# Performance work log

Hardware: AMD Instinct MI355X
Metric: run time of the kernel (lower is better)

## Reference

```python
import jax, jax.numpy as jnp
import numpy as np

H = 19  # input_size == hidden_size

def setup_inputs() -> dict:
    key = jax.random.key(0)
    ks = jax.random.split(key, 7)
    seq_len, batch = 2048, 1024
    s = 1.0 / np.sqrt(H)  # PyTorch default uniform(-1/sqrt(H), 1/sqrt(H))
    x = jax.random.normal(ks[0], (seq_len, batch, H), dtype=jnp.float32)
    W_ih = jax.random.uniform(ks[1], (3 * H, H), jnp.float32, -s, s)
    W_hh = jax.random.uniform(ks[2], (3 * H, H), jnp.float32, -s, s)
    b_ih = jax.random.uniform(ks[3], (3 * H,), jnp.float32, -s, s)
    b_hh = jax.random.uniform(ks[4], (3 * H,), jnp.float32, -s, s)
    W_out = jax.random.uniform(ks[5], (1, H), jnp.float32, -s, s)
    b_out = jax.random.uniform(ks[6], (1,), jnp.float32, -s, s)
    return {"x": x, "W_ih": W_ih, "W_hh": W_hh, "b_ih": b_ih,
            "b_hh": b_hh, "W_out": W_out, "b_out": b_out}

def _gru(x, W_ih, W_hh, b_ih, b_hh):
    # Precompute all input projections in one big GEMM: [T, B, 3H]
    xg = jnp.einsum('tbi,gi->tbg', x, W_ih) + b_ih
    Whr, Whz, Whn = W_hh[:H], W_hh[H:2*H], W_hh[2*H:]
    bhr, bhz, bhn = b_hh[:H], b_hh[H:2*H], b_hh[2*H:]
    h0 = jnp.zeros(x.shape[1:2] + (H,), dtype=x.dtype)

    def step(h, xg_t):
        xr, xz, xn = xg_t[:, :H], xg_t[:, H:2*H], xg_t[:, 2*H:]
        r = jax.nn.sigmoid(xr + h @ Whr.T + bhr)
        z = jax.nn.sigmoid(xz + h @ Whz.T + bhz)
        n = jnp.tanh(xn + r * (h @ Whn.T + bhn))
        h_new = (1.0 - z) * n + z * h
        return h_new, h_new

    _, r_out = jax.lax.scan(step, h0, xg)  # r_out: [T, B, H]
    return r_out

def reference(x, W_ih, W_hh, b_ih, b_hh, W_out, b_out):
    r_out = _gru(x, W_ih, W_hh, b_ih, b_hh)
    return r_out @ W_out.T + b_out  # [T, B, 1]
```

## Files before the change

### kernel.cpp

```cpp
#include <hip/hip_runtime.h>
#include <math.h>

#define HH 19
#define NB 1024
#define TT 2048

typedef float v2f __attribute__((ext_vector_type(2)));
typedef unsigned u2 __attribute__((ext_vector_type(2)));

__device__ __forceinline__ float rlf(float v, int l) {
  return __uint_as_float(__builtin_amdgcn_readlane(__float_as_uint(v), l));
}
__device__ __forceinline__ float frcp(float v) {
  return __builtin_amdgcn_rcpf(v);
}
__device__ __forceinline__ float fexp2(float v) {
#if __has_builtin(__builtin_amdgcn_exp2f)
  return __builtin_amdgcn_exp2f(v);
#else
  return exp2f(v);
#endif
}
__device__ __forceinline__ v2f vfma(v2f a, v2f b, v2f c) {
#if __has_builtin(__builtin_elementwise_fma)
  return __builtin_elementwise_fma(a, b, c);
#else
  v2f r; r.x = fmaf(a.x, b.x, c.x); r.y = fmaf(a.y, b.y, c.y); return r;
#endif
}

#if __has_builtin(__builtin_amdgcn_permlane32_swap)
#define HAVE_PLS 1
__device__ __forceinline__ u2 pls(float x) {
  unsigned u = __float_as_uint(x);
  return __builtin_amdgcn_permlane32_swap(u, u, false, false);
}
#else
#define HAVE_PLS 0
#endif

__global__ void __launch_bounds__(64)
__attribute__((amdgpu_waves_per_eu(1, 1)))
gru57_v4(const float* __restrict__ x, const float* __restrict__ Wih,
         const float* __restrict__ Whh, const float* __restrict__ bih,
         const float* __restrict__ bhh, const float* __restrict__ Wout,
         const float* __restrict__ bout, float* __restrict__ out)
{
  const int b = blockIdx.x;
  const int lane = threadIdx.x;

  const float L2E = 1.4426950408889634f;

  int row;
  if (lane < 32)      row = lane;
  else if (lane < 51) row = lane + 6;
  else if (lane < 57) row = lane - 19;
  else                row = 37;
  const bool isn = (row >= 2 * HH);
  const float scale = isn ? (2.0f * L2E) : L2E;

  v2f wx2[10], wh2[10], wo2[10];
#pragma unroll
  for (int j = 0; j < 10; ++j) {
    const int k0 = 2 * j, k1 = 2 * j + 1;
    wx2[j].x = Wih[row * HH + k0] * scale;
    wx2[j].y = (k1 < HH) ? Wih[row * HH + k1] * scale : 0.0f;
    wh2[j].x = Whh[row * HH + k0] * scale;
    wh2[j].y = (k1 < HH) ? Whh[row * HH + k1] * scale : 0.0f;
    wo2[j].x = Wout[k0];
    wo2[j].y = (k1 < HH) ? Wout[k1] : 0.0f;
  }
  const float bxv = bih[row] * scale, bhv = bhh[row] * scale;
  const float ax0 = isn ? bxv : (bxv + bhv);
  const float ah0 = isn ? bhv : 0.0f;
  const float bo  = bout[0];

  const int il = lane < HH ? lane : HH - 1;
  const int zaddr = ((il < 13) ? (19 + il) : (38 + il)) * 4;

#if HAVE_PLS
  bool loIsX;
  {
    unsigned l = (unsigned)lane;
    u2 pr = __builtin_amdgcn_permlane32_swap(l, l, false, false);
    loIsX = ((unsigned)__builtin_amdgcn_readlane((int)pr.x, 32) < 32u);
  }
#else
  const int loaddr = (lane & 31) * 4;
  const int hiaddr = ((lane & 31) | 32) * 4;
#endif

  float h = 0.0f;
  v2f sh2[10];
#pragma unroll
  for (int j = 0; j < 10; ++j) { sh2[j].x = 0.0f; sh2[j].y = 0.0f; }

  const int kx = lane < HH ? lane : HH - 1;
  const float* __restrict__ xbase = x + (size_t)b * HH + kx;

#define LOADX(dst, trow) do {                                           \
    dst = xbase[(size_t)(trow) * (NB * HH)];                            \
  } while (0)

#define XBCAST(slot, xu) do {                                           \
    _Pragma("unroll")                                                   \
    for (int _j = 0; _j < 9; ++_j) {                                    \
      xu[_j].x = rlf(slot, 2 * _j);                                     \
      xu[_j].y = rlf(slot, 2 * _j + 1);                                 \
    }                                                                   \
    xu[9].x = rlf(slot, 18); xu[9].y = 0.0f;                            \
  } while (0)

#define XDOT(xu, dstvar) do {                                           \
    v2f _aA = {ax0, 0.0f}, _aB = {0.0f, 0.0f};                          \
    _Pragma("unroll")                                                   \
    for (int _j = 0; _j < 5; ++_j)  _aA = vfma(xu[_j], wx2[_j], _aA);   \
    _Pragma("unroll")                                                   \
    for (int _j = 5; _j < 10; ++_j) _aB = vfma(xu[_j], wx2[_j], _aB);   \
    const v2f _s = _aA + _aB;                                           \
    dstvar = _s.x + _s.y;                                               \
  } while (0)

#if HAVE_PLS
#define LOBCAST(val, dst) do { u2 _s = pls(val);                        \
    dst = __uint_as_float(loIsX ? _s.x : _s.y); } while (0)
#define HIBCAST(val, dst) do { u2 _s = pls(val);                        \
    dst = __uint_as_float(loIsX ? _s.y : _s.x); } while (0)
#else
#define LOBCAST(val, dst) dst = __uint_as_float((unsigned)              \
    __builtin_amdgcn_ds_bpermute(loaddr, (int)__float_as_uint(val)))
#define HIBCAST(val, dst) dst = __uint_as_float((unsigned)              \
    __builtin_amdgcn_ds_bpermute(hiaddr, (int)__float_as_uint(val)))
#endif

  float xlA, xlB, xlC, xlD;
  LOADX(xlA, 0); LOADX(xlB, 1); LOADX(xlC, 2); LOADX(xlD, 3);

  float prex;
  {
    v2f xu0[10];
    XBCAST(xlA, xu0);
    XDOT(xu0, prex);
  }

#define BODY(tcur, nslot, lslot) do {                                   \
                 \
    v2f ahA = {ah0, 0.0f}, ahB = {0.0f, 0.0f};                          \
    _Pragma("unroll")                                                   \
    for (int _j = 0; _j < 5; ++_j)  ahA = vfma(sh2[_j], wh2[_j], ahA);  \
    _Pragma("unroll")                                                   \
    for (int _j = 5; _j < 10; ++_j) ahB = vfma(sh2[_j], wh2[_j], ahB);  \
               \
    float prexN;                                                        \
    { v2f _xu[10];                                                      \
      XBCAST(nslot, _xu);                                               \
      XDOT(_xu, prexN); }                                               \
    { const int _tl = ((tcur) + 4 < TT) ? (tcur) + 4 : TT - 1;          \
      LOADX(lslot, _tl); }                                              \
                                                   \
    const v2f ahv = ahA + ahB;                                          \
    const float preh = ahv.x + ahv.y;                                   \
    const float pre  = prex + preh;                                     \
    const float sig  = frcp(1.0f + fexp2(-pre));                        \
    const int zzi = __builtin_amdgcn_ds_bpermute(                       \
        zaddr, (int)__float_as_uint(sig));                              \
    float rr; LOBCAST(sig, rr);                                         \
    const float npre = fmaf(rr, preh, prex);                            \
    const float nn = fmaf(-2.0f, frcp(fexp2(npre) + 1.0f), 1.0f);       \
    float nh; HIBCAST(nn, nh);                                          \
    const float zz = __uint_as_float((unsigned)zzi);                    \
    h = fmaf(zz, h - nh, nh);                                           \
                  \
    _Pragma("unroll")                                                   \
    for (int _j = 0; _j < 9; ++_j) {                                    \
      sh2[_j].x = rlf(h, 2 * _j);                                       \
      sh2[_j].y = rlf(h, 2 * _j + 1);                                   \
    }                                                                   \
    sh2[9].x = rlf(h, 18); sh2[9].y = 0.0f;                             \
        \
    v2f oA = {bo, 0.0f}, oB = {0.0f, 0.0f};                             \
    _Pragma("unroll")                                                   \
    for (int _j = 0; _j < 5; ++_j)  oA = vfma(sh2[_j], wo2[_j], oA);    \
    _Pragma("unroll")                                                   \
    for (int _j = 5; _j < 10; ++_j) oB = vfma(sh2[_j], wo2[_j], oB);    \
    const v2f ov = oA + oB;                                             \
    if (lane == 0) out[(size_t)(tcur) * NB + b] = ov.x + ov.y;          \
    prex = prexN;                                                       \
  } while (0)

  for (int t = 0; t < TT; t += 4) {
    BODY(t + 0, xlB, xlA);
    BODY(t + 1, xlC, xlB);
    BODY(t + 2, xlD, xlC);
    BODY(t + 3, xlA, xlD);
  }

#undef LOADX
#undef XBCAST
#undef XDOT
#undef BODY
#undef LOBCAST
#undef HIBCAST
}

extern "C" void kernel_launch(void* const* d_in, const int* in_sizes, int n_in,
                              void* d_out, int out_size, void* d_ws, size_t ws_size,
                              hipStream_t stream) {
  const float* x    = (const float*)d_in[0];
  const float* Wih  = (const float*)d_in[1];
  const float* Whh  = (const float*)d_in[2];
  const float* bih  = (const float*)d_in[3];
  const float* bhh  = (const float*)d_in[4];
  const float* Wout = (const float*)d_in[5];
  const float* bout = (const float*)d_in[6];
  float* out = (float*)d_out;

  gru57_v4<<<dim3(NB), dim3(64), 0, stream>>>(
      x, Wih, Whh, bih, bhh, Wout, bout, out);
}
```

Before: 555.2 us.

## Split input projection into separate fp16 precompute kernel before recurrence

Adds a parallel kernel that computes all input-gate projections for every timestep and batch element and stores them as fp16 in the workspace. The recurrent kernel then loads one precomputed half value per lane per step, which takes the per-step x broadcast and x-dot-product off the serial loop; its prefetch depth grows to 8 steps. The cost is an extra launch and a large intermediate write and read (about 240 MB of fp16). Storing the projections in fp16 also loses precision. The original fused kernel is kept as a fallback when the workspace is too small.

```diff
diff --git a/kernel.cpp b/kernel.cpp
--- a/kernel.cpp
+++ b/kernel.cpp
@@ -2,24 +2,31 @@
 #include <math.h>
 
 #define HH 19
+#define NG 57
+#define GP 20
 #define NB 1024
 #define TT 2048
 
+typedef float v4f __attribute__((ext_vector_type(4)));
+typedef unsigned u2 __attribute__((ext_vector_type(2)));
 typedef float v2f __attribute__((ext_vector_type(2)));
-typedef unsigned u2 __attribute__((ext_vector_type(2)));
 
 __device__ __forceinline__ float rlf(float v, int l) {
   return __uint_as_float(__builtin_amdgcn_readlane(__float_as_uint(v), l));
 }
-__device__ __forceinline__ float frcp(float v) {
-  return __builtin_amdgcn_rcpf(v);
-}
+__device__ __forceinline__ float frcp(float v) { return __builtin_amdgcn_rcpf(v); }
 __device__ __forceinline__ float fexp2(float v) {
 #if __has_builtin(__builtin_amdgcn_exp2f)
   return __builtin_amdgcn_exp2f(v);
 #else
   return exp2f(v);
 #endif
+}
+__device__ __forceinline__ unsigned short f2h(float f) {
+  return __builtin_bit_cast(unsigned short, (_Float16)f);
+}
+__device__ __forceinline__ float h2f(unsigned short u) {
+  return (float)__builtin_bit_cast(_Float16, u);
 }
 __device__ __forceinline__ v2f vfma(v2f a, v2f b, v2f c) {
 #if __has_builtin(__builtin_elementwise_fma)
@@ -38,6 +45,161 @@
 #else
 #define HAVE_PLS 0
 #endif
+
+__global__ __launch_bounds__(256) void xg_proj(
+    const float* __restrict__ x, const float* __restrict__ Wih,
+    const float* __restrict__ bih, const float* __restrict__ bhh,
+    unsigned short* __restrict__ xg)
+{
+  __shared__ __align__(16) float wl[NG][GP];
+  __shared__ float cb[NG];
+  const float L2E = 1.4426950408889634f;
+  for (int idx = threadIdx.x; idx < NG * GP; idx += 256) {
+    const int g = idx / GP, k = idx - g * GP;
+    const float s = (g < 2 * HH) ? L2E : 2.0f * L2E;
+    wl[g][k] = (k < HH) ? Wih[g * HH + k] * s : 0.0f;
+  }
+  if (threadIdx.x < NG) {
+    const int g = threadIdx.x;
+    const float s = (g < 2 * HH) ? L2E : 2.0f * L2E;
+    cb[g] = (bih[g] + (g < 2 * HH ? bhh[g] : 0.0f)) * s;
+  }
+  __syncthreads();
+
+  const size_t tid = (size_t)blockIdx.x * 256 + threadIdx.x;
+  const float* __restrict__ xr = x + tid * HH;
+  float xv[GP];
+#pragma unroll
+  for (int k = 0; k < HH; ++k) xv[k] = xr[k];
+  xv[HH] = 0.0f;
+
+  unsigned short* __restrict__ o = xg + tid * NG;
+#pragma unroll 3
+  for (int g = 0; g < NG; ++g) {
+    float a = cb[g];
+#pragma unroll
+    for (int q = 0; q < GP; q += 4) {
+      const v4f w = *(const v4f*)&wl[g][q];
+      a = fmaf(xv[q + 0], w.x, a);
+      a = fmaf(xv[q + 1], w.y, a);
+      a = fmaf(xv[q + 2], w.z, a);
+      a = fmaf(xv[q + 3], w.w, a);
+    }
+    o[g] = f2h(a);
+  }
+}
+
+__global__ void __launch_bounds__(64)
+__attribute__((amdgpu_waves_per_eu(1, 1)))
+gru_rec(const unsigned short* __restrict__ xg, const float* __restrict__ Whh,
+        const float* __restrict__ bhh, const float* __restrict__ Wout,
+        const float* __restrict__ bout, float* __restrict__ out)
+{
+  const int b = blockIdx.x;
+  const int lane = threadIdx.x;
+  const float L2E = 1.4426950408889634f;
+
+  int row;
+  if (lane < 32)      row = lane;
+  else if (lane < 51) row = lane + 6;
+  else if (lane < 57) row = lane - 19;
+  else                row = 37;
+  const bool isn = (row >= 2 * HH);
+  const float scale = isn ? (2.0f * L2E) : L2E;
+
+  float wh[HH], wo[HH];
+#pragma unroll
+  for (int k = 0; k < HH; ++k) {
+    wh[k] = Whh[row * HH + k] * scale;
+    wo[k] = Wout[k];
+  }
+  const float ah0 = isn ? bhh[row] * scale : 0.0f;
+  const float bo  = bout[0];
+
+  const int il = lane < HH ? lane : HH - 1;
+  const int zaddr = ((il < 13) ? (19 + il) : (38 + il)) * 4;
+
+#if HAVE_PLS
+  bool loIsX;
+  {
+    unsigned l = (unsigned)lane;
+    u2 pr = __builtin_amdgcn_permlane32_swap(l, l, false, false);
+    loIsX = ((unsigned)__builtin_amdgcn_readlane((int)pr.x, 32) < 32u);
+  }
+#define LOBCAST(val, dst) do { u2 _s = pls(val);                        \
+    dst = __uint_as_float(loIsX ? _s.x : _s.y); } while (0)
+#define HIBCAST(val, dst) do { u2 _s = pls(val);                        \
+    dst = __uint_as_float(loIsX ? _s.y : _s.x); } while (0)
+#else
+  const int loaddr = (lane & 31) * 4;
+  const int hiaddr = ((lane & 31) | 32) * 4;
+#define LOBCAST(val, dst) dst = __uint_as_float((unsigned)              \
+    __builtin_amdgcn_ds_bpermute(loaddr, (int)__float_as_uint(val)))
+#define HIBCAST(val, dst) dst = __uint_as_float((unsigned)              \
+    __builtin_amdgcn_ds_bpermute(hiaddr, (int)__float_as_uint(val)))
+#endif
+
+  float h = 0.0f;
+  float sh[HH];
+#pragma unroll
+  for (int k = 0; k < HH; ++k) sh[k] = 0.0f;
+
+  const unsigned short* __restrict__ xb = xg + (size_t)b * NG + row;
+
+#define LOADX(dst, trow) do {                                           \
+    dst = xb[(size_t)(trow) * (NB * NG)];                               \
+  } while (0)
+
+  unsigned short s0, s1, s2, s3, s4, s5, s6, s7;
+  LOADX(s0, 0); LOADX(s1, 1); LOADX(s2, 2); LOADX(s3, 3);
+  LOADX(s4, 4); LOADX(s5, 5); LOADX(s6, 6); LOADX(s7, 7);
+
+#define BODY(tcur, slot) do {                                           \
+    const float xv = h2f(slot);                                         \
+    float a0 = ah0, a1 = 0.0f, a2 = 0.0f, a3 = 0.0f;                    \
+    _Pragma("unroll")                                                   \
+    for (int _k = 0; _k < HH; ++_k) {                                   \
+      if ((_k & 3) == 0) a0 = fmaf(sh[_k], wh[_k], a0);                 \
+      if ((_k & 3) == 1) a1 = fmaf(sh[_k], wh[_k], a1);                 \
+      if ((_k & 3) == 2) a2 = fmaf(sh[_k], wh[_k], a2);                 \
+      if ((_k & 3) == 3) a3 = fmaf(sh[_k], wh[_k], a3);                 \
+    }                                                                   \
+    const float preh = (a0 + a1) + (a2 + a3);                           \
+    const float pre  = xv + preh;                                       \
+    const float sig  = frcp(1.0f + fexp2(-pre));                        \
+    const int zzi = __builtin_amdgcn_ds_bpermute(                       \
+        zaddr, (int)__float_as_uint(sig));                              \
+    float rr; LOBCAST(sig, rr);                                         \
+    const float npre = fmaf(rr, preh, xv);                              \
+    const float nn = fmaf(-2.0f, frcp(fexp2(npre) + 1.0f), 1.0f);       \
+    float nh; HIBCAST(nn, nh);                                          \
+    const float zz = __uint_as_float((unsigned)zzi);                    \
+    h = fmaf(zz, h - nh, nh);                                           \
+    _Pragma("unroll")                                                   \
+    for (int _k = 0; _k < HH; ++_k) sh[_k] = rlf(h, _k);                \
+    float o0 = bo, o1 = 0.0f, o2 = 0.0f, o3 = 0.0f;                     \
+    _Pragma("unroll")                                                   \
+    for (int _k = 0; _k < HH; ++_k) {                                   \
+      if ((_k & 3) == 0) o0 = fmaf(sh[_k], wo[_k], o0);                 \
+      if ((_k & 3) == 1) o1 = fmaf(sh[_k], wo[_k], o1);                 \
+      if ((_k & 3) == 2) o2 = fmaf(sh[_k], wo[_k], o2);                 \
+      if ((_k & 3) == 3) o3 = fmaf(sh[_k], wo[_k], o3);                 \
+    }                                                                   \
+    if (lane == 0) out[(size_t)(tcur) * NB + b] = (o0 + o1) + (o2 + o3);\
+    { const int _tl = ((tcur) + 8 < TT) ? (tcur) + 8 : TT - 1;          \
+      LOADX(slot, _tl); }                                               \
+  } while (0)
+
+  for (int t = 0; t < TT; t += 8) {
+    BODY(t + 0, s0); BODY(t + 1, s1); BODY(t + 2, s2); BODY(t + 3, s3);
+    BODY(t + 4, s4); BODY(t + 5, s5); BODY(t + 6, s6); BODY(t + 7, s7);
+  }
+
+#undef LOADX
+#undef BODY
+#undef LOBCAST
+#undef HIBCAST
+}
 
 __global__ void __launch_bounds__(64)
 __attribute__((amdgpu_waves_per_eu(1, 1)))
@@ -48,7 +210,6 @@
 {
   const int b = blockIdx.x;
   const int lane = threadIdx.x;
-
   const float L2E = 1.4426950408889634f;
 
   int row;
@@ -85,9 +246,17 @@
     u2 pr = __builtin_amdgcn_permlane32_swap(l, l, false, false);
     loIsX = ((unsigned)__builtin_amdgcn_readlane((int)pr.x, 32) < 32u);
   }
+#define LOBCAST(val, dst) do { u2 _s = pls(val);                        \
+    dst = __uint_as_float(loIsX ? _s.x : _s.y); } while (0)
+#define HIBCAST(val, dst) do { u2 _s = pls(val);                        \
+    dst = __uint_as_float(loIsX ? _s.y : _s.x); } while (0)
 #else
   const int loaddr = (lane & 31) * 4;
   const int hiaddr = ((lane & 31) | 32) * 4;
+#define LOBCAST(val, dst) dst = __uint_as_float((unsigned)              \
+    __builtin_amdgcn_ds_bpermute(loaddr, (int)__float_as_uint(val)))
+#define HIBCAST(val, dst) dst = __uint_as_float((unsigned)              \
+    __builtin_amdgcn_ds_bpermute(hiaddr, (int)__float_as_uint(val)))
 #endif
 
   float h = 0.0f;
@@ -98,10 +267,7 @@
   const int kx = lane < HH ? lane : HH - 1;
   const float* __restrict__ xbase = x + (size_t)b * HH + kx;
 
-#define LOADX(dst, trow) do {                                           \
-    dst = xbase[(size_t)(trow) * (NB * HH)];                            \
-  } while (0)
-
+#define LOADXF(dst, trow) do { dst = xbase[(size_t)(trow) * (NB * HH)]; } while (0)
 #define XBCAST(slot, xu) do {                                           \
     _Pragma("unroll")                                                   \
     for (int _j = 0; _j < 9; ++_j) {                                    \
@@ -110,7 +276,6 @@
     }                                                                   \
     xu[9].x = rlf(slot, 18); xu[9].y = 0.0f;                            \
   } while (0)
-
 #define XDOT(xu, dstvar) do {                                           \
     v2f _aA = {ax0, 0.0f}, _aB = {0.0f, 0.0f};                          \
     _Pragma("unroll")                                                   \
@@ -121,43 +286,21 @@
     dstvar = _s.x + _s.y;                                               \
   } while (0)
 
-#if HAVE_PLS
-#define LOBCAST(val, dst) do { u2 _s = pls(val);                        \
-    dst = __uint_as_float(loIsX ? _s.x : _s.y); } while (0)
-#define HIBCAST(val, dst) do { u2 _s = pls(val);                        \
-    dst = __uint_as_float(loIsX ? _s.y : _s.x); } while (0)
-#else
-#define LOBCAST(val, dst) dst = __uint_as_float((unsigned)              \
-    __builtin_amdgcn_ds_bpermute(loaddr, (int)__float_as_uint(val)))
-#define HIBCAST(val, dst) dst = __uint_as_float((unsigned)              \
-    __builtin_amdgcn_ds_bpermute(hiaddr, (int)__float_as_uint(val)))
-#endif
-
   float xlA, xlB, xlC, xlD;
-  LOADX(xlA, 0); LOADX(xlB, 1); LOADX(xlC, 2); LOADX(xlD, 3);
-
+  LOADXF(xlA, 0); LOADXF(xlB, 1); LOADXF(xlC, 2); LOADXF(xlD, 3);
   float prex;
-  {
-    v2f xu0[10];
-    XBCAST(xlA, xu0);
-    XDOT(xu0, prex);
-  }
-
-#define BODY(tcur, nslot, lslot) do {                                   \
-                 \
+  { v2f xu0[10]; XBCAST(xlA, xu0); XDOT(xu0, prex); }
+
+#define BODYF(tcur, nslot, lslot) do {                                  \
     v2f ahA = {ah0, 0.0f}, ahB = {0.0f, 0.0f};                          \
     _Pragma("unroll")                                                   \
     for (int _j = 0; _j < 5; ++_j)  ahA = vfma(sh2[_j], wh2[_j], ahA);  \
     _Pragma("unroll")                                                   \
     for (int _j = 5; _j < 10; ++_j) ahB = vfma(sh2[_j], wh2[_j], ahB);  \
-               \
     float prexN;                                                        \
-    { v2f _xu[10];                                                      \
-      XBCAST(nslot, _xu);                                               \
-      XDOT(_xu, prexN); }                                               \
+    { v2f _xu[10]; XBCAST(nslot, _xu); XDOT(_xu, prexN); }              \
     { const int _tl = ((tcur) + 4 < TT) ? (tcur) + 4 : TT - 1;          \
-      LOADX(lslot, _tl); }                                              \
-                                                   \
+      LOADXF(lslot, _tl); }                                             \
     const v2f ahv = ahA + ahB;                                          \
     const float preh = ahv.x + ahv.y;                                   \
     const float pre  = prex + preh;                                     \
@@ -170,14 +313,12 @@
     float nh; HIBCAST(nn, nh);                                          \
     const float zz = __uint_as_float((unsigned)zzi);                    \
     h = fmaf(zz, h - nh, nh);                                           \
-                  \
     _Pragma("unroll")                                                   \
     for (int _j = 0; _j < 9; ++_j) {                                    \
       sh2[_j].x = rlf(h, 2 * _j);                                       \
       sh2[_j].y = rlf(h, 2 * _j + 1);                                   \
     }                                                                   \
     sh2[9].x = rlf(h, 18); sh2[9].y = 0.0f;                             \
-        \
     v2f oA = {bo, 0.0f}, oB = {0.0f, 0.0f};                             \
     _Pragma("unroll")                                                   \
     for (int _j = 0; _j < 5; ++_j)  oA = vfma(sh2[_j], wo2[_j], oA);    \
@@ -189,16 +330,16 @@
   } while (0)
 
   for (int t = 0; t < TT; t += 4) {
-    BODY(t + 0, xlB, xlA);
-    BODY(t + 1, xlC, xlB);
-    BODY(t + 2, xlD, xlC);
-    BODY(t + 3, xlA, xlD);
-  }
-
-#undef LOADX
+    BODYF(t + 0, xlB, xlA);
+    BODYF(t + 1, xlC, xlB);
+    BODYF(t + 2, xlD, xlC);
+    BODYF(t + 3, xlA, xlD);
+  }
+
+#undef LOADXF
 #undef XBCAST
 #undef XDOT
-#undef BODY
+#undef BODYF
 #undef LOBCAST
 #undef HIBCAST
 }
@@ -215,6 +356,15 @@
   const float* bout = (const float*)d_in[6];
   float* out = (float*)d_out;
 
-  gru57_v4<<<dim3(NB), dim3(64), 0, stream>>>(
-      x, Wih, Whh, bih, bhh, Wout, bout, out);
-}
+  const size_t need = (size_t)TT * NB * NG * sizeof(unsigned short);
+  if (ws_size >= need) {
+    unsigned short* xgws = (unsigned short*)d_ws;
+    xg_proj<<<dim3((TT * NB) / 256), dim3(256), 0, stream>>>(
+        x, Wih, bih, bhh, xgws);
+    gru_rec<<<dim3(NB), dim3(64), 0, stream>>>(
+        xgws, Whh, bhh, Wout, bout, out);
+  } else {
+    gru57_v4<<<dim3(NB), dim3(64), 0, stream>>>(
+        x, Wih, Whh, bih, bhh, Wout, bout, out);
+  }
+}
```

After: 837.2 us. 1.51x slower.

## Split GRU into fp16 input-projection pass and lane-per-hidden recurrence kernel

Applied to the files above, without the earlier changes.

Adds a separate kernel that precomputes the scaled input projections for all timesteps and stores them in fp16 in the workspace. A new recurrence kernel then assigns one lane per hidden unit, computing all three gates in that lane. It broadcasts h through shared memory with vector loads instead of 19 readlanes, and drops the cross-lane permutes for r, z and n. This takes the x·W_ih dot product and its broadcasts off the serial per-step critical path. In exchange it adds a large workspace write and read, fp16 rounding of the preactivations, and more FMAs per lane.

```diff
diff --git a/kernel.cpp b/kernel.cpp
--- a/kernel.cpp
+++ b/kernel.cpp
@@ -2,18 +2,18 @@
 #include <math.h>
 
 #define HH 19
+#define NG 57
 #define NB 1024
 #define TT 2048
 
 typedef float v2f __attribute__((ext_vector_type(2)));
+typedef float v4f __attribute__((ext_vector_type(4)));
 typedef unsigned u2 __attribute__((ext_vector_type(2)));
 
 __device__ __forceinline__ float rlf(float v, int l) {
   return __uint_as_float(__builtin_amdgcn_readlane(__float_as_uint(v), l));
 }
-__device__ __forceinline__ float frcp(float v) {
-  return __builtin_amdgcn_rcpf(v);
-}
+__device__ __forceinline__ float frcp(float v) { return __builtin_amdgcn_rcpf(v); }
 __device__ __forceinline__ float fexp2(float v) {
 #if __has_builtin(__builtin_amdgcn_exp2f)
   return __builtin_amdgcn_exp2f(v);
@@ -21,6 +21,13 @@
   return exp2f(v);
 #endif
 }
+__device__ __forceinline__ unsigned short f2h(float f) {
+  return __builtin_bit_cast(unsigned short, (_Float16)f);
+}
+__device__ __forceinline__ float h2f(unsigned short u) {
+  return (float)__builtin_bit_cast(_Float16, u);
+}
+__device__ __forceinline__ v2f mk2(float a, float b) { v2f r; r.x = a; r.y = b; return r; }
 __device__ __forceinline__ v2f vfma(v2f a, v2f b, v2f c) {
 #if __has_builtin(__builtin_elementwise_fma)
   return __builtin_elementwise_fma(a, b, c);
@@ -38,6 +45,166 @@
 #else
 #define HAVE_PLS 0
 #endif
+
+__global__ __launch_bounds__(256) void xg_proj2(
+    const float* __restrict__ x, const float* __restrict__ Wih,
+    const float* __restrict__ bih, const float* __restrict__ bhh,
+    unsigned short* __restrict__ xg)
+{
+  const int lane = threadIdx.x & 63;
+  const int wv = __builtin_amdgcn_readfirstlane((int)(threadIdx.x >> 6));
+  const int g = lane < NG ? lane : NG - 1;
+  const float L2E = 1.4426950408889634f;
+  const float scale = (g < 2 * HH) ? -L2E : 2.0f * L2E;
+
+  float w[HH];
+#pragma unroll
+  for (int k = 0; k < HH; ++k) w[k] = Wih[g * HH + k] * scale;
+  const float cbv = (bih[g] + (g < 2 * HH ? bhh[g] : 0.0f)) * scale;
+
+  const size_t pair0 = ((size_t)blockIdx.x * 4 + wv) * 64;
+  for (int p = 0; p < 64; ++p) {
+    const size_t pair = pair0 + p;
+    const float* __restrict__ xr = x + pair * HH;
+    float a = cbv;
+#pragma unroll
+    for (int k = 0; k < HH; ++k) a = fmaf(xr[k], w[k], a);
+    if (lane < NG) xg[pair * NG + g] = f2h(a);
+  }
+}
+
+__global__ void __launch_bounds__(64)
+__attribute__((amdgpu_waves_per_eu(1, 1)))
+gru_rec2(const unsigned short* __restrict__ xg, const float* __restrict__ Whh,
+         const float* __restrict__ bhh, const float* __restrict__ Wout,
+         const float* __restrict__ bout, float* __restrict__ out)
+{
+  __shared__ __align__(16) float hsh[64];
+  const int b = blockIdx.x;
+  const int lane = threadIdx.x;
+  const int i = lane < HH ? lane : HH - 1;
+  const float L2E = 1.4426950408889634f;
+
+  v2f wr2[10], wz2[10], wn2[10], wo2[10];
+#pragma unroll
+  for (int j = 0; j < 10; ++j) {
+    const int k0 = 2 * j, k1 = 2 * j + 1;
+    wr2[j].x = -L2E * Whh[i * HH + k0];
+    wr2[j].y = (k1 < HH) ? -L2E * Whh[i * HH + k1] : 0.0f;
+    wz2[j].x = -L2E * Whh[(HH + i) * HH + k0];
+    wz2[j].y = (k1 < HH) ? -L2E * Whh[(HH + i) * HH + k1] : 0.0f;
+    wn2[j].x = 2.0f * L2E * Whh[(2 * HH + i) * HH + k0];
+    wn2[j].y = (k1 < HH) ? 2.0f * L2E * Whh[(2 * HH + i) * HH + k1] : 0.0f;
+    wo2[j].x = Wout[k0];
+    wo2[j].y = (k1 < HH) ? Wout[k1] : 0.0f;
+  }
+  const float bnv = 2.0f * L2E * bhh[2 * HH + i];
+  const float bo = bout[0];
+
+  float h = 0.0f;
+
+  const unsigned short* __restrict__ xb = xg + (size_t)b * NG;
+#define LR(dst, t) dst = xb[(size_t)(t) * (NB * NG) + i]
+#define LZ(dst, t) dst = xb[(size_t)(t) * (NB * NG) + HH + i]
+#define LN(dst, t) dst = xb[(size_t)(t) * (NB * NG) + 2 * HH + i]
+
+  unsigned short r0,r1,r2,r3,r4,r5,r6,r7;
+  unsigned short z0,z1,z2,z3,z4,z5,z6,z7;
+  unsigned short n0,n1,n2,n3,n4,n5,n6,n7;
+  LR(r0,0); LZ(z0,0); LN(n0,0);  LR(r1,1); LZ(z1,1); LN(n1,1);
+  LR(r2,2); LZ(z2,2); LN(n2,2);  LR(r3,3); LZ(z3,3); LN(n3,3);
+  LR(r4,4); LZ(z4,4); LN(n4,4);  LR(r5,5); LZ(z5,5); LN(n5,5);
+  LR(r6,6); LZ(z6,6); LN(n6,6);  LR(r7,7); LZ(z7,7); LN(n7,7);
+
+#define BODY(tcur, rs, zs, ns) do {                                      \
+              \
+    hsh[lane] = (lane < HH) ? h : 0.0f;                                  \
+    const v4f q0 = *(const v4f*)&hsh[0];                                 \
+    const v4f q1 = *(const v4f*)&hsh[4];                                 \
+    const v4f q2 = *(const v4f*)&hsh[8];                                 \
+    const v4f q3 = *(const v4f*)&hsh[12];                                \
+    const v4f q4 = *(const v4f*)&hsh[16];                                \
+    v2f sh2[10];                                                         \
+    sh2[0]=mk2(q0.x,q0.y); sh2[1]=mk2(q0.z,q0.w);                        \
+    sh2[2]=mk2(q1.x,q1.y); sh2[3]=mk2(q1.z,q1.w);                        \
+    sh2[4]=mk2(q2.x,q2.y); sh2[5]=mk2(q2.z,q2.w);                        \
+    sh2[6]=mk2(q3.x,q3.y); sh2[7]=mk2(q3.z,q3.w);                        \
+    sh2[8]=mk2(q4.x,q4.y); sh2[9]=mk2(q4.z,q4.w);                        \
+                        \
+    v2f oA = mk2(bo, 0.0f), oB = mk2(0.0f, 0.0f);                        \
+    _Pragma("unroll")                                                    \
+    for (int _j = 0; _j < 5; ++_j)  oA = vfma(sh2[_j], wo2[_j], oA);     \
+    _Pragma("unroll")                                                    \
+    for (int _j = 5; _j < 10; ++_j) oB = vfma(sh2[_j], wo2[_j], oB);     \
+    const v2f ov = oA + oB;                                              \
+    if (lane == 0) {                                                     \
+      const int tp = (tcur) > 0 ? (tcur) - 1 : 0;                        \
+      out[(size_t)tp * NB + b] = ov.x + ov.y;                            \
+    }                                                                    \
+                     \
+    const float xvr = h2f(rs), xvz = h2f(zs), xvn = h2f(ns);             \
+    v2f aR0 = mk2(xvr, 0.0f), aR1 = mk2(0.0f, 0.0f);                     \
+    v2f aZ0 = mk2(xvz, 0.0f), aZ1 = mk2(0.0f, 0.0f);                     \
+    v2f aN0 = mk2(bnv, 0.0f), aN1 = mk2(0.0f, 0.0f);                     \
+    _Pragma("unroll")                                                    \
+    for (int _j = 0; _j < 5; ++_j) {                                     \
+      aR0 = vfma(sh2[_j], wr2[_j], aR0);                                 \
+      aZ0 = vfma(sh2[_j], wz2[_j], aZ0);                                 \
+      aN0 = vfma(sh2[_j], wn2[_j], aN0);                                 \
+    }                                                                    \
+    _Pragma("unroll")                                                    \
+    for (int _j = 5; _j < 10; ++_j) {                                    \
+      aR1 = vfma(sh2[_j], wr2[_j], aR1);                                 \
+      aZ1 = vfma(sh2[_j], wz2[_j], aZ1);                                 \
+      aN1 = vfma(sh2[_j], wn2[_j], aN1);                                 \
+    }                                                                    \
+    const v2f mR = aR0 + aR1, mZ = aZ0 + aZ1, mN = aN0 + aN1;            \
+    const float preR = mR.x + mR.y;            \
+    const float preZ = mZ.x + mZ.y;            \
+    const float preN = mN.x + mN.y;          \
+    const float rr = frcp(fexp2(preR) + 1.0f);              \
+    const float zz = frcp(fexp2(preZ) + 1.0f);                           \
+    const float argP = fmaf(rr, preN, xvn);           \
+    const float D = frcp(fexp2(argP) + 1.0f);                            \
+    const float nn = fmaf(-2.0f, D, 1.0f);               \
+    h = fmaf(zz, h - nn, nn);                                            \
+    { const int tl = ((tcur) + 8 < TT) ? (tcur) + 8 : TT - 1;            \
+      LR(rs, tl); LZ(zs, tl); LN(ns, tl); }                              \
+  } while (0)
+
+  for (int t = 0; t < TT; t += 8) {
+    BODY(t + 0, r0, z0, n0); BODY(t + 1, r1, z1, n1);
+    BODY(t + 2, r2, z2, n2); BODY(t + 3, r3, z3, n3);
+    BODY(t + 4, r4, z4, n4); BODY(t + 5, r5, z5, n5);
+    BODY(t + 6, r6, z6, n6); BODY(t + 7, r7, z7, n7);
+  }
+
+  hsh[lane] = (lane < HH) ? h : 0.0f;
+  {
+    const v4f q0 = *(const v4f*)&hsh[0];
+    const v4f q1 = *(const v4f*)&hsh[4];
+    const v4f q2 = *(const v4f*)&hsh[8];
+    const v4f q3 = *(const v4f*)&hsh[12];
+    const v4f q4 = *(const v4f*)&hsh[16];
+    v2f sh2[10];
+    sh2[0]=mk2(q0.x,q0.y); sh2[1]=mk2(q0.z,q0.w);
+    sh2[2]=mk2(q1.x,q1.y); sh2[3]=mk2(q1.z,q1.w);
+    sh2[4]=mk2(q2.x,q2.y); sh2[5]=mk2(q2.z,q2.w);
+    sh2[6]=mk2(q3.x,q3.y); sh2[7]=mk2(q3.z,q3.w);
+    sh2[8]=mk2(q4.x,q4.y); sh2[9]=mk2(q4.z,q4.w);
+    v2f oA = mk2(bo, 0.0f), oB = mk2(0.0f, 0.0f);
+#pragma unroll
+    for (int j = 0; j < 5; ++j)  oA = vfma(sh2[j], wo2[j], oA);
+#pragma unroll
+    for (int j = 5; j < 10; ++j) oB = vfma(sh2[j], wo2[j], oB);
+    const v2f ov = oA + oB;
+    if (lane == 0) out[(size_t)(TT - 1) * NB + b] = ov.x + ov.y;
+  }
+#undef LR
+#undef LZ
+#undef LN
+#undef BODY
+}
 
 __global__ void __launch_bounds__(64)
 __attribute__((amdgpu_waves_per_eu(1, 1)))
@@ -48,7 +215,6 @@
 {
   const int b = blockIdx.x;
   const int lane = threadIdx.x;
-
   const float L2E = 1.4426950408889634f;
 
   int row;
@@ -85,9 +251,17 @@
     u2 pr = __builtin_amdgcn_permlane32_swap(l, l, false, false);
     loIsX = ((unsigned)__builtin_amdgcn_readlane((int)pr.x, 32) < 32u);
   }
+#define LOBCAST(val, dst) do { u2 _s = pls(val);                        \
+    dst = __uint_as_float(loIsX ? _s.x : _s.y); } while (0)
+#define HIBCAST(val, dst) do { u2 _s = pls(val);                        \
+    dst = __uint_as_float(loIsX ? _s.y : _s.x); } while (0)
 #else
   const int loaddr = (lane & 31) * 4;
   const int hiaddr = ((lane & 31) | 32) * 4;
+#define LOBCAST(val, dst) dst = __uint_as_float((unsigned)              \
+    __builtin_amdgcn_ds_bpermute(loaddr, (int)__float_as_uint(val)))
+#define HIBCAST(val, dst) dst = __uint_as_float((unsigned)              \
+    __builtin_amdgcn_ds_bpermute(hiaddr, (int)__float_as_uint(val)))
 #endif
 
   float h = 0.0f;
@@ -98,10 +272,7 @@
   const int kx = lane < HH ? lane : HH - 1;
   const float* __restrict__ xbase = x + (size_t)b * HH + kx;
 
-#define LOADX(dst, trow) do {                                           \
-    dst = xbase[(size_t)(trow) * (NB * HH)];                            \
-  } while (0)
-
+#define LOADXF(dst, trow) do { dst = xbase[(size_t)(trow) * (NB * HH)]; } while (0)
 #define XBCAST(slot, xu) do {                                           \
     _Pragma("unroll")                                                   \
     for (int _j = 0; _j < 9; ++_j) {                                    \
@@ -110,9 +281,8 @@
     }                                                                   \
     xu[9].x = rlf(slot, 18); xu[9].y = 0.0f;                            \
   } while (0)
-
 #define XDOT(xu, dstvar) do {                                           \
-    v2f _aA = {ax0, 0.0f}, _aB = {0.0f, 0.0f};                          \
+    v2f _aA = mk2(ax0, 0.0f), _aB = mk2(0.0f, 0.0f);                    \
     _Pragma("unroll")                                                   \
     for (int _j = 0; _j < 5; ++_j)  _aA = vfma(xu[_j], wx2[_j], _aA);   \
     _Pragma("unroll")                                                   \
@@ -121,43 +291,21 @@
     dstvar = _s.x + _s.y;                                               \
   } while (0)
 
-#if HAVE_PLS
-#define LOBCAST(val, dst) do { u2 _s = pls(val);                        \
-    dst = __uint_as_float(loIsX ? _s.x : _s.y); } while (0)
-#define HIBCAST(val, dst) do { u2 _s = pls(val);                        \
-    dst = __uint_as_float(loIsX ? _s.y : _s.x); } while (0)
-#else
-#define LOBCAST(val, dst) dst = __uint_as_float((unsigned)              \
-    __builtin_amdgcn_ds_bpermute(loaddr, (int)__float_as_uint(val)))
-#define HIBCAST(val, dst) dst = __uint_as_float((unsigned)              \
-    __builtin_amdgcn_ds_bpermute(hiaddr, (int)__float_as_uint(val)))
-#endif
-
   float xlA, xlB, xlC, xlD;
-  LOADX(xlA, 0); LOADX(xlB, 1); LOADX(xlC, 2); LOADX(xlD, 3);
-
+  LOADXF(xlA, 0); LOADXF(xlB, 1); LOADXF(xlC, 2); LOADXF(xlD, 3);
   float prex;
-  {
-    v2f xu0[10];
-    XBCAST(xlA, xu0);
-    XDOT(xu0, prex);
-  }
-
-#define BODY(tcur, nslot, lslot) do {                                   \
-                 \
-    v2f ahA = {ah0, 0.0f}, ahB = {0.0f, 0.0f};                          \
+  { v2f xu0[10]; XBCAST(xlA, xu0); XDOT(xu0, prex); }
+
+#define BODYF(tcur, nslot, lslot) do {                                  \
+    v2f ahA = mk2(ah0, 0.0f), ahB = mk2(0.0f, 0.0f);                    \
     _Pragma("unroll")                                                   \
     for (int _j = 0; _j < 5; ++_j)  ahA = vfma(sh2[_j], wh2[_j], ahA);  \
     _Pragma("unroll")                                                   \
     for (int _j = 5; _j < 10; ++_j) ahB = vfma(sh2[_j], wh2[_j], ahB);  \
-               \
     float prexN;                                                        \
-    { v2f _xu[10];                                                      \
-      XBCAST(nslot, _xu);                                               \
-      XDOT(_xu, prexN); }                                               \
+    { v2f _xu[10]; XBCAST(nslot, _xu); XDOT(_xu, prexN); }              \
     { const int _tl = ((tcur) + 4 < TT) ? (tcur) + 4 : TT - 1;          \
-      LOADX(lslot, _tl); }                                              \
-                                                   \
+      LOADXF(lslot, _tl); }                                             \
     const v2f ahv = ahA + ahB;                                          \
     const float preh = ahv.x + ahv.y;                                   \
     const float pre  = prex + preh;                                     \
@@ -170,15 +318,13 @@
     float nh; HIBCAST(nn, nh);                                          \
     const float zz = __uint_as_float((unsigned)zzi);                    \
     h = fmaf(zz, h - nh, nh);                                           \
-                  \
     _Pragma("unroll")                                                   \
     for (int _j = 0; _j < 9; ++_j) {                                    \
       sh2[_j].x = rlf(h, 2 * _j);                                       \
       sh2[_j].y = rlf(h, 2 * _j + 1);                                   \
     }                                                                   \
     sh2[9].x = rlf(h, 18); sh2[9].y = 0.0f;                             \
-        \
-    v2f oA = {bo, 0.0f}, oB = {0.0f, 0.0f};                             \
+    v2f oA = mk2(bo, 0.0f), oB = mk2(0.0f, 0.0f);                       \
     _Pragma("unroll")                                                   \
     for (int _j = 0; _j < 5; ++_j)  oA = vfma(sh2[_j], wo2[_j], oA);    \
     _Pragma("unroll")                                                   \
@@ -189,16 +335,16 @@
   } while (0)
 
   for (int t = 0; t < TT; t += 4) {
-    BODY(t + 0, xlB, xlA);
-    BODY(t + 1, xlC, xlB);
-    BODY(t + 2, xlD, xlC);
-    BODY(t + 3, xlA, xlD);
-  }
-
-#undef LOADX
+    BODYF(t + 0, xlB, xlA);
+    BODYF(t + 1, xlC, xlB);
+    BODYF(t + 2, xlD, xlC);
+    BODYF(t + 3, xlA, xlD);
+  }
+
+#undef LOADXF
 #undef XBCAST
 #undef XDOT
-#undef BODY
+#undef BODYF
 #undef LOBCAST
 #undef HIBCAST
 }
@@ -215,6 +361,15 @@
   const float* bout = (const float*)d_in[6];
   float* out = (float*)d_out;
 
-  gru57_v4<<<dim3(NB), dim3(64), 0, stream>>>(
-      x, Wih, Whh, bih, bhh, Wout, bout, out);
-}
+  const size_t need = (size_t)TT * NB * NG * sizeof(unsigned short);
+  if (ws_size >= need) {
+    unsigned short* xgws = (unsigned short*)d_ws;
+    xg_proj2<<<dim3((TT * NB) / 256), dim3(256), 0, stream>>>(
+        x, Wih, bih, bhh, xgws);
+    gru_rec2<<<dim3(NB), dim3(64), 0, stream>>>(
+        xgws, Whh, bhh, Wout, bout, out);
+  } else {
+    gru57_v4<<<dim3(NB), dim3(64), 0, stream>>>(
+        x, Wih, Whh, bih, bhh, Wout, bout, out);
+  }
+}
```

Measured after the change: 688.4 us. 1.24x slower.
